# Performance work log

Hardware: AMD Instinct MI355X
Metric: run time of the kernel (lower is better)

Reference implementation:

```python
import jax, jax.numpy as jnp
import numpy as np

D_MODEL = 512
D_KEY = 512
D_VALUE = 512
DEG = 2                      # poly_degree
C = 16                       # context_window
D_POLY = (DEG + 1) * D_KEY   # 1536
MAX_NORM = 50.0
EPS = 1e-6
BATCH, SEQ = 8, 2048


def poly_features(x, coeffs):
    # phi(x) = concat_i coeffs[i] * x**i, i = 0..DEG   [..., (DEG+1)*d]
    outs = []
    xp = jnp.ones_like(x)
    for i in range(DEG + 1):
        outs.append(coeffs[i] * xp)
        xp = xp * x
    return jnp.concatenate(outs, axis=-1)


def _xavier(key, shape):
    fan_in, fan_out = shape[1], shape[0]
    lim = np.sqrt(6.0 / (fan_in + fan_out))
    return jax.random.uniform(key, shape, jnp.float32, -lim, lim)


def _logit(p):
    return float(np.log(p / (1.0 - p)))


def setup_inputs() -> dict:
    key = jax.random.key(0)
    ks = jax.random.split(key, 12)
    x = jax.random.normal(ks[0], (BATCH, SEQ, D_MODEL), jnp.float32)
    M0 = jnp.zeros((BATCH, D_POLY, D_VALUE), jnp.float32)
    S0 = jnp.zeros((BATCH, D_POLY, D_VALUE), jnp.float32)
    coeffs = jnp.array([1.0, 1.0, 0.5], jnp.float32)  # 1/i!
    return {
        "x": x, "M0": M0, "S0": S0,
        "Wk": _xavier(ks[1], (D_KEY, D_MODEL)),
        "Wv": _xavier(ks[2], (D_VALUE, D_MODEL)),
        "Wq": _xavier(ks[3], (D_KEY, D_MODEL)),
        "Wqk": jnp.eye(D_KEY, dtype=jnp.float32),
        "Wout": _xavier(ks[4], (D_MODEL, D_VALUE)),
        "coeffs": coeffs,
        "cgWq": _xavier(ks[5], (D_MODEL, D_MODEL)),
        "cgWk": _xavier(ks[6], (D_MODEL, D_MODEL)),
        "temp": jnp.ones((1,), jnp.float32),
        "aw": 0.01 * jax.random.normal(ks[7], (1, D_MODEL), jnp.float32),
        "ab": jnp.full((1,), _logit(0.99), jnp.float32),
        "tw": 0.01 * jax.random.normal(ks[8], (1, D_MODEL), jnp.float32),
        "tb": jnp.full((1,), _logit(0.9), jnp.float32),
        "ew": 0.01 * jax.random.normal(ks[9], (1, D_MODEL), jnp.float32),
        "eb": jnp.full((1,), _logit(0.1), jnp.float32),
    }


def _forward(x, M0, S0, Wk, Wv, Wq, Wqk, Wout, coeffs,
             cgWq, cgWk, temp, aw, ab, tw, tb, ew, eb):
    B, S, _ = x.shape
    n_chunks = S // C
    xc = x.reshape(B, n_chunks, C, D_MODEL).transpose(1, 0, 2, 3)  # [n,B,C,d]
    inv_temp = 1.0 / (D_MODEL ** 0.5 * jnp.maximum(temp[0], 0.1))

    def step(carry, chunk):
        M, Smom = carry                       # [B, d_poly, d_value]
        k = chunk @ Wk.T                      # [B,C,d_key]
        phi = poly_features(k, coeffs)        # [B,C,d_poly]
        v = chunk @ Wv.T                      # [B,C,d_value]
        # context gates from the current (last) token of the chunk
        qg = chunk[:, -1] @ cgWq.T            # [B,d]
        kg = chunk @ cgWk.T                   # [B,C,d]
        gamma = jax.nn.sigmoid(jnp.einsum('bcd,bd->bc', kg, qg) * inv_temp)
        # input-dependent alpha/theta/eta (mean-pooled chunk)
        xm = chunk.mean(axis=1)               # [B,d]
        alpha = jax.nn.sigmoid(xm @ aw.T + ab)[:, :, None]  # [B,1,1]
        theta = jax.nn.sigmoid(xm @ tw.T + tb)[:, :, None]
        eta = jax.nn.sigmoid(xm @ ew.T + eb)[:, :, None]
        # omega gradient: 2/C * Phi^T (Gamma (Phi M - V))
        pred = jnp.einsum('bcp,bpv->bcv', phi, M)
        err = gamma[..., None] * (pred - v)
        grad = (2.0 / C) * jnp.einsum('bcp,bcv->bpv', phi, err)
        S_new = theta * Smom - eta * grad
        M_new = alpha * M + S_new
        norms = jnp.sqrt(jnp.sum(M_new * M_new, axis=(-2, -1), keepdims=True))
        M_new = M_new * jnp.minimum(MAX_NORM / (norms + EPS), 1.0)
        # memory updates are detached by design (online learning inside scan)
        M_new = jax.lax.stop_gradient(M_new)
        S_new = jax.lax.stop_gradient(S_new)
        # read with polynomial-expanded query
        q = (chunk @ Wq.T) @ Wqk.T
        phiq = poly_features(q, coeffs)
        y = jnp.einsum('bcp,bpv->bcv', phiq, M_new) @ Wout.T
        return (M_new, S_new), y

    (_, _), ys = jax.lax.scan(step, (M0, S0), xc)   # ys: [n,B,C,d_model]
    return ys.transpose(1, 0, 2, 3).reshape(B, S, D_MODEL)


def reference(x, M0, S0, Wk, Wv, Wq, Wqk, Wout, coeffs,
              cgWq, cgWk, temp, aw, ab, tw, tb, ew, eb):
    return _forward(x, M0, S0, Wk, Wv, Wq, Wqk, Wout, coeffs,
                    cgWq, cgWk, temp, aw, ab, tw, tb, ew, eb)
```

## Files before the change

### kernel.cpp

```cpp
#include <hip/hip_runtime.h>
#include <hip/hip_bf16.h>
#include <math.h>

typedef __attribute__((ext_vector_type(4))) float f32x4;
typedef __attribute__((ext_vector_type(8))) short bf16x8;
typedef unsigned short u16;
typedef unsigned int u32;
typedef unsigned long long u64;

__device__ __forceinline__ float bf2f(u16 h){
  u32 u = ((u32)h) << 16;
  return __builtin_bit_cast(float, u);
}
__device__ __forceinline__ u16 f2bf(float f){
  u32 u = __builtin_bit_cast(u32, f);
  u32 r = (u + 0x7FFFu + ((u >> 16) & 1u)) >> 16;
  return (u16)r;
}
__device__ __forceinline__ float ldany(const void* p, long i, int f32){
  return f32 ? ((const float*)p)[i] : bf2f(((const u16*)p)[i]);
}

#define MFMA16(A, B, C) __builtin_amdgcn_mfma_f32_16x16x32_bf16(A, B, C, 0, 0, 0)
#define MM6(acc, AH, AM, AL, BH, BM, BL) \
  acc = MFMA16(AH, BH, acc); acc = MFMA16(AH, BM, acc); acc = MFMA16(AM, BH, acc); \
  acc = MFMA16(AM, BM, acc); acc = MFMA16(AL, BH, acc); acc = MFMA16(AH, BL, acc);

__global__ void detect_kernel(const u32* __restrict__ wqk_raw, int* __restrict__ flag){
  *flag = (wqk_raw[0] == 0x3F800000u) ? 1 : 0;
}

__global__ __launch_bounds__(512) void cvt_scalars_kernel(
    const void* temp, const void* aw, const void* ab, const void* tw, const void* tb,
    const void* ew, const void* eb, const void* coeffs, float* __restrict__ scal,
    const int* __restrict__ flag){
  int f = *flag; int d = threadIdx.x;
  scal[1 + d]    = ldany(aw, d, f);
  scal[514 + d]  = ldany(tw, d, f);
  scal[1027 + d] = ldany(ew, d, f);
  if (d == 0){
    scal[0]    = ldany(temp, 0, f);
    scal[513]  = ldany(ab, 0, f);
    scal[1026] = ldany(tb, 0, f);
    scal[1539] = ldany(eb, 0, f);
    scal[1540] = ldany(coeffs, 0, f);
    scal[1541] = ldany(coeffs, 1, f);
    scal[1542] = ldany(coeffs, 2, f);
  }
}

__global__ __launch_bounds__(256) void trans_kernel(
    const void* __restrict__ W, float* __restrict__ WT, const int* __restrict__ flag){
  int f = *flag;
  int idx = blockIdx.x * 256 + threadIdx.x;
  WT[idx] = ldany(W, (long)(idx & 511) * 512 + (idx >> 9), f);
}

__global__ __launch_bounds__(256) void split_kernel(
    const void* __restrict__ src, int srcmode, long n,
    u16* __restrict__ h, u16* __restrict__ m, u16* __restrict__ l,
    const int* __restrict__ flag){
  long i = (long)blockIdx.x * 256 + threadIdx.x;
  if (i >= n) return;
  int f = srcmode ? 1 : *flag;
  float v = ldany(src, i, f);
  u16 a = f2bf(v); float r1 = v - bf2f(a);
  u16 bq = f2bf(r1);
  h[i] = a; m[i] = bq; l[i] = f2bf(r1 - bf2f(bq));
}

__global__ __launch_bounds__(256) void gemm6(
    const u16* __restrict__ Ah, const u16* __restrict__ Am, const u16* __restrict__ Al,
    long a_off, int a_stride,
    const u16* __restrict__ Bh, const u16* __restrict__ Bm, const u16* __restrict__ Bl,
    void* __restrict__ OUT, int out_stride, int out_mode, const int* __restrict__ flag)
{
  const int rt = blockIdx.x;
  const int w = threadIdx.x >> 6, lane = threadIdx.x & 63;
  const int lm = lane & 15, quad = lane >> 4;
  const int col0 = blockIdx.y * 64 + w * 16;
  const long abase = a_off + (long)(rt * 16 + lm) * a_stride + quad * 8;
  const long bbase = (long)(col0 + lm) * 512 + quad * 8;
  f32x4 acc = {0.f, 0.f, 0.f, 0.f};
#pragma unroll
  for (int kk = 0; kk < 16; kk++){
    bf16x8 AH = *(const bf16x8*)(Ah + abase + kk * 32);
    bf16x8 AM = *(const bf16x8*)(Am + abase + kk * 32);
    bf16x8 AL = *(const bf16x8*)(Al + abase + kk * 32);
    bf16x8 BH = *(const bf16x8*)(Bh + bbase + kk * 32);
    bf16x8 BM = *(const bf16x8*)(Bm + bbase + kk * 32);
    bf16x8 BL = *(const bf16x8*)(Bl + bbase + kk * 32);
    MM6(acc, AH, AM, AL, BH, BM, BL)
  }
  const int orow = rt * 16 + quad * 4;
  const int f32out = (out_mode == 1) ? 1 : *flag;
#pragma unroll
  for (int r = 0; r < 4; r++){
    long o = (long)(orow + r) * out_stride + col0 + lm;
    if (f32out) ((float*)OUT)[o] = acc[r];
    else        ((u16*)OUT)[o]   = f2bf(acc[r]);
  }
}

__global__ __launch_bounds__(256) void gemm6s(
    const u16* __restrict__ Ah, const u16* __restrict__ Am, const u16* __restrict__ Al,
    long a_off, int a_stride,
    const u16* __restrict__ Bh, const u16* __restrict__ Bm, const u16* __restrict__ Bl,
    void* __restrict__ OUT, int out_stride, int out_mode,
    int rows_band, int cg, const int* __restrict__ flag)
{
  const int id = blockIdx.x;
  const int xcd = id & 7;
  const int s = id >> 3;
  const int per_grp = rows_band * cg;
  const int cgi = s / per_grp;
  const int t = s - cgi * per_grp;
  const int rt = xcd * rows_band + t / cg;
  const int ct = cgi * cg + (t - (t / cg) * cg);

  const int w = threadIdx.x >> 6, lane = threadIdx.x & 63;
  const int lm = lane & 15, quad = lane >> 4;
  const int col0 = ct * 64 + w * 16;
  const long abase = a_off + (long)(rt * 16 + lm) * a_stride + quad * 8;
  const long bbase = (long)(col0 + lm) * 512 + quad * 8;
  f32x4 acc = {0.f, 0.f, 0.f, 0.f};
#pragma unroll
  for (int kk = 0; kk < 16; kk++){
    bf16x8 AH = *(const bf16x8*)(Ah + abase + kk * 32);
    bf16x8 AM = *(const bf16x8*)(Am + abase + kk * 32);
    bf16x8 AL = *(const bf16x8*)(Al + abase + kk * 32);
    bf16x8 BH = *(const bf16x8*)(Bh + bbase + kk * 32);
    bf16x8 BM = *(const bf16x8*)(Bm + bbase + kk * 32);
    bf16x8 BL = *(const bf16x8*)(Bl + bbase + kk * 32);
    MM6(acc, AH, AM, AL, BH, BM, BL)
  }
  const int orow = rt * 16 + quad * 4;
  const int f32out = (out_mode == 1) ? 1 : *flag;
#pragma unroll
  for (int r = 0; r < 4; r++){
    long o = (long)(orow + r) * out_stride + col0 + lm;
    if (f32out) ((float*)OUT)[o] = acc[r];
    else        ((u16*)OUT)[o]   = f2bf(acc[r]);
  }
}

__global__ __launch_bounds__(256) void gamma_ate_kernel(
    const void* __restrict__ x, const float* __restrict__ z,
    const float* __restrict__ scal, const int* __restrict__ flag,
    float* __restrict__ gammaO, float* __restrict__ ateO)
{
  int bn = blockIdx.x;
  int tid = threadIdx.x;
  int f = *flag;
  __shared__ float gred[16][17];
  __shared__ float red[256];

  float t0 = scal[0];
  float mt = t0 > 0.1f ? t0 : 0.1f;
  float it = 1.0f / (22.627416997969522f * mt);

  int c = tid >> 4, part = tid & 15;
  long xrb = ((long)bn * 16 + c) * 512 + part * 32;
  const float* zr = z + (long)bn * 512 + part * 32;
  float p = 0.f;
  for (int e = 0; e < 32; e++) p += ldany(x, xrb + e, f) * zr[e];
  gred[c][part] = p;
  __syncthreads();
  if (tid < 16){
    float s = 0.f;
    for (int q2 = 0; q2 < 16; q2++) s += gred[tid][q2];
    gammaO[bn * 16 + tid] = 1.f / (1.f + expf(-it * s));
  }

  long xbase = (long)bn * 16 * 512;
  int d = tid * 2;
  float x0 = 0.f, x1 = 0.f;
  for (int cc = 0; cc < 16; cc++){
    x0 += ldany(x, xbase + cc * 512 + d, f);
    x1 += ldany(x, xbase + cc * 512 + d + 1, f);
  }
  x0 *= 0.0625f; x1 *= 0.0625f;
  float pa = x0 * scal[1 + d]    + x1 * scal[1 + d + 1];
  float pt = x0 * scal[514 + d]  + x1 * scal[514 + d + 1];
  float pe = x0 * scal[1027 + d] + x1 * scal[1027 + d + 1];

  red[tid] = pa; __syncthreads();
  for (int o = 128; o > 0; o >>= 1){ if (tid < o) red[tid] += red[tid + o]; __syncthreads(); }
  if (tid == 0) ateO[bn * 3 + 0] = 1.f / (1.f + expf(-(red[0] + scal[513])));
  __syncthreads();
  red[tid] = pt; __syncthreads();
  for (int o = 128; o > 0; o >>= 1){ if (tid < o) red[tid] += red[tid + o]; __syncthreads(); }
  if (tid == 0) ateO[bn * 3 + 1] = 1.f / (1.f + expf(-(red[0] + scal[1026])));
  __syncthreads();
  red[tid] = pe; __syncthreads();
  for (int o = 128; o > 0; o >>= 1){ if (tid < o) red[tid] += red[tid + o]; __syncthreads(); }
  if (tid == 0) ateO[bn * 3 + 2] = 1.f / (1.f + expf(-(red[0] + scal[1539])));
}

__device__ __forceinline__ void acc16f(const float4* k4, float c1M, float c2M,
                                       float pp[16]){
  float4 a = k4[0], b = k4[1], c = k4[2], d = k4[3];
  float kv[16] = {a.x,a.y,a.z,a.w, b.x,b.y,b.z,b.w, c.x,c.y,c.z,c.w, d.x,d.y,d.z,d.w};
#pragma unroll
  for (int i = 0; i < 16; i++){
    float t = c1M + kv[i] * c2M;
    pp[i] += kv[i] * t;
  }
}
__device__ __forceinline__ void grad16(const float4* k4, const float er[16],
                                       float& g1, float& g2){
  float4 a = k4[0], b = k4[1], c = k4[2], d = k4[3];
  float kv[16] = {a.x,a.y,a.z,a.w, b.x,b.y,b.z,b.w, c.x,c.y,c.z,c.w, d.x,d.y,d.z,d.w};
  float s1a = 0.f, s1b = 0.f, s2a = 0.f, s2b = 0.f;
#pragma unroll
  for (int i = 0; i < 16; i += 2){
    float ta = kv[i] * er[i];
    float tb = kv[i + 1] * er[i + 1];
    s1a += ta; s1b += tb;
    s2a += kv[i] * ta; s2b += kv[i + 1] * tb;
  }
  g1 = s1a + s1b; g2 = s2a + s2b;
}

__global__ __launch_bounds__(512, 2) void scan_kernel(
    const float* __restrict__ KVQ,
    const float* __restrict__ gammaA, const float* __restrict__ ateA,
    const float* __restrict__ scal,
    const void* __restrict__ M0, const void* __restrict__ S0,
    const int* __restrict__ flag,
    float* __restrict__ YT, u64* ssE)
{
  const int b = blockIdx.x >> 5;
  const int jt = blockIdx.x & 31, j0 = jt * 16;
  const int tid = threadIdx.x;
  const int g = tid >> 4, j = tid & 15, col = j0 + j;
  const int w = tid >> 6, lane = tid & 63;

  __shared__ float bufQ[512 * 16];
  __shared__ float bufK[512 * 16];
  __shared__ float redY[256 * 33];
  __shared__ float redP[256 * 33];
  __shared__ float errL[16 * 17];
  __shared__ float sprevS;
  __shared__ float ssw[8];

  const float c0f = scal[1540], c1f = scal[1541], c2f = scal[1542];
  const int f = *flag;

  float M[48], S[48];
  if (f){
#pragma unroll
    for (int k = 0; k < 48; k++){
      long gi = ((long)(b * 1536 + (k >> 4) * 512 + g + 32 * (k & 15))) * 512 + col;
      M[k] = ((const float*)M0)[gi];
      S[k] = ((const float*)S0)[gi];
    }
  } else {
#pragma unroll
    for (int k = 0; k < 48; k++){
      long gi = ((long)(b * 1536 + (k >> 4) * 512 + g + 32 * (k & 15))) * 512 + col;
      M[k] = bf2f(((const u16*)M0)[gi]);
      S[k] = bf2f(((const u16*)S0)[gi]);
    }
  }

  const int cS = tid & 15;
  const int dS = (tid >> 4) * 16;

  float4 k0, k1, k2, k3, q0, q1, q2, q3;
  {
    const float* ks = KVQ + ((long)(b * 2048 + cS)) * 1536 + dS;
    k0 = *(const float4*)(ks);     k1 = *(const float4*)(ks + 4);
    k2 = *(const float4*)(ks + 8); k3 = *(const float4*)(ks + 12);
  }
  q0 = k0; q1 = k1; q2 = k2; q3 = k3;

#pragma unroll 1
  for (int n = 0; n <= 128; n++){
    if (n > 0){
      float* bp = &bufQ[dS * 16 + cS];
      bp[0]   = q0.x; bp[16]  = q0.y; bp[32]  = q0.z; bp[48]  = q0.w;
      bp[64]  = q1.x; bp[80]  = q1.y; bp[96]  = q1.z; bp[112] = q1.w;
      bp[128] = q2.x; bp[144] = q2.y; bp[160] = q2.z; bp[176] = q2.w;
      bp[192] = q3.x; bp[208] = q3.y; bp[224] = q3.z; bp[240] = q3.w;
    }
    if (n < 128){
      float* bp = &bufK[dS * 16 + cS];
      bp[0]   = k0.x; bp[16]  = k0.y; bp[32]  = k0.z; bp[48]  = k0.w;
      bp[64]  = k1.x; bp[80]  = k1.y; bp[96]  = k1.z; bp[112] = k1.w;
      bp[128] = k2.x; bp[144] = k2.y; bp[160] = k2.z; bp[176] = k2.w;
      bp[192] = k3.x; bp[208] = k3.y; bp[224] = k3.z; bp[240] = k3.w;
    }
    __syncthreads();

    float vv = 0.f, gam = 0.f, alpha = 0.f, theta = 0.f, eta = 0.f;
    if (n < 128){
      const float* qs = KVQ + ((long)(b * 2048 + n * 16 + cS)) * 1536 + 1024 + dS;
      q0 = *(const float4*)(qs);     q1 = *(const float4*)(qs + 4);
      q2 = *(const float4*)(qs + 8); q3 = *(const float4*)(qs + 12);
      if (n < 127){
        const float* ks = KVQ + ((long)(b * 2048 + (n + 1) * 16 + cS)) * 1536 + dS;
        k0 = *(const float4*)(ks);     k1 = *(const float4*)(ks + 4);
        k2 = *(const float4*)(ks + 8); k3 = *(const float4*)(ks + 12);
      }
      if (tid >= 256){
        int idx = tid - 256, c2 = idx >> 4, j2 = idx & 15;
        vv  = KVQ[((long)(b * 2048 + n * 16 + c2)) * 1536 + 512 + j0 + j2];
        gam = gammaA[(b * 128 + n) * 16 + c2];
      }
      alpha = ateA[(b * 128 + n) * 3 + 0];
      theta = ateA[(b * 128 + n) * 3 + 1];
      eta   = ateA[(b * 128 + n) * 3 + 2];
    }

    float bsum = 0.f;
#pragma unroll
    for (int m = 0; m < 16; m++) bsum += M[m];
    const float base0 = c0f * bsum;

    {
      float pp[16];
#pragma unroll
      for (int c = 0; c < 16; c++) pp[c] = 0.f;
#pragma unroll
      for (int m = 0; m < 16; m++)
        acc16f((const float4*)&bufQ[g * 16 + m * 512],
               c1f * M[16 + m], c2f * M[32 + m], pp);
#pragma unroll
      for (int c = 0; c < 16; c++)
        redY[(c * 16 + j) * 33 + g] = base0 + pp[c];
    }
    {
      float pp[16];
#pragma unroll
      for (int c = 0; c < 16; c++) pp[c] = 0.f;
#pragma unroll
      for (int m = 0; m < 16; m++)
        acc16f((const float4*)&bufK[g * 16 + m * 512],
               c1f * M[16 + m], c2f * M[32 + m], pp);
#pragma unroll
      for (int c = 0; c < 16; c++)
        redP[(c * 16 + j) * 33 + g] = base0 + pp[c];
    }

    if (n > 0 && tid < 64){
      float ssv = 0.f;
      if (tid < 32){
        const u64* sp = ssE + ((n - 1) & 1) * 256 + b * 32;
        u64 v;
        for (;;){
          v = __hip_atomic_load(&sp[tid], __ATOMIC_RELAXED, __HIP_MEMORY_SCOPE_AGENT);
          if ((u32)(v >> 32) >= (u32)n) break;
          __builtin_amdgcn_s_sleep(1);
        }
        ssv = __builtin_bit_cast(float, (u32)(v & 0xFFFFFFFFu));
      }
#pragma unroll
      for (int o = 16; o > 0; o >>= 1) ssv += __shfl_xor(ssv, o);
      if (tid == 0) sprevS = fminf(50.0f / (sqrtf(ssv) + 1e-6f), 1.0f);
    }
    __syncthreads();
    const float s_prev = (n > 0) ? sprevS : 1.0f;

    if (tid < 256){
      if (n > 0){
        int c2 = tid >> 4, j2 = tid & 15;
        const float* rp = &redY[(c2 * 16 + j2) * 33];
        float yt = 0.f;
#pragma unroll
        for (int i = 0; i < 32; i++) yt += rp[i];
        YT[((long)(b * 2048 + (n - 1) * 16 + c2)) * 512 + j0 + j2] = s_prev * yt;
      }
    } else {
      if (n < 128){
        int idx = tid - 256, c2 = idx >> 4, j2 = idx & 15;
        const float* rp = &redP[(c2 * 16 + j2) * 33];
        float pred = 0.f;
#pragma unroll
        for (int i = 0; i < 32; i++) pred += rp[i];
        errL[c2 * 17 + j2] = 0.125f * gam * (s_prev * pred - vv);
      }
    }
    __syncthreads();

    if (n < 128){
      const float alphaS = alpha * s_prev;
      float er[16];
#pragma unroll
      for (int c = 0; c < 16; c++) er[c] = errL[c * 17 + j];
      float g0 = 0.f;
#pragma unroll
      for (int c = 0; c < 16; c++) g0 += er[c];
      float lss = 0.f;
#pragma unroll
      for (int m = 0; m < 16; m++){
        float g1, g2;
        grad16((const float4*)&bufK[g * 16 + m * 512], er, g1, g2);
        float sn1 = theta * S[16 + m] - eta * (c1f * g1);
        float an1 = alphaS * M[16 + m] + sn1;
        S[16 + m] = sn1; M[16 + m] = an1; lss += an1 * an1;
        float sn2 = theta * S[32 + m] - eta * (c2f * g2);
        float an2 = alphaS * M[32 + m] + sn2;
        S[32 + m] = sn2; M[32 + m] = an2; lss += an2 * an2;
      }
      float gv0 = eta * (c0f * g0);
#pragma unroll
      for (int m = 0; m < 16; m++){
        float sn = theta * S[m] - gv0;
        float an = alphaS * M[m] + sn;
        S[m] = sn; M[m] = an; lss += an * an;
      }
#pragma unroll
      for (int off2 = 32; off2 > 0; off2 >>= 1) lss += __shfl_down(lss, off2);
      if (lane == 0) ssw[w] = lss;
    }
    __syncthreads();
    if (n < 128 && tid == 0){
      float tot = ssw[0] + ssw[1] + ssw[2] + ssw[3]
                + ssw[4] + ssw[5] + ssw[6] + ssw[7];
      u64 pv = ((u64)(u32)(n + 1) << 32) | (u64)__builtin_bit_cast(u32, tot);
      __hip_atomic_store(&ssE[(n & 1) * 256 + b * 32 + jt], pv,
                         __ATOMIC_RELAXED, __HIP_MEMORY_SCOPE_AGENT);
    }
  }
}

extern "C" void kernel_launch(void* const* d_in, const int* in_sizes, int n_in,
                              void* d_out, int out_size, void* d_ws, size_t ws_size,
                              hipStream_t stream)
{
  (void)in_sizes; (void)n_in; (void)out_size;
  const void* x      = d_in[0];
  const void* M0     = d_in[1];
  const void* S0     = d_in[2];
  const void* Wk     = d_in[3];
  const void* Wv     = d_in[4];
  const void* Wq     = d_in[5];
  const void* Wqk    = d_in[6];
  const void* Wout   = d_in[7];
  const void* coeffs = d_in[8];
  const void* cgWq   = d_in[9];
  const void* cgWk   = d_in[10];
  const void* temp   = d_in[11];
  const void* aw     = d_in[12];
  const void* ab     = d_in[13];
  const void* tw     = d_in[14];
  const void* tb     = d_in[15];
  const void* ew     = d_in[16];
  const void* eb     = d_in[17];

  char* ws = (char*)d_ws;
  size_t off = 0;
  float* KVQ32 = (float*)(ws + off); off += 100663296;
  char*  XR  = ws + off;           off += 50331648;
  u16* Wsp   = (u16*)(ws + off);   off += 9437184;
  float* qg32  = (float*)(ws + off); off += 2097152;
  u16*   qgs   = (u16*)(ws + off);   off += 3145728;
  float* Wq2f  = (float*)(ws + off); off += 1048576;
  float* cgWkT = (float*)(ws + off); off += 1048576;
  float* z32   = (float*)(ws + off); off += 2097152;
  float* scal_  = (float*)(ws + off); off += 8192;
  float* gamma_ = (float*)(ws + off); off += 65536;
  float* ate_   = (float*)(ws + off); off += 12288;
  u64* ssE_     = (u64*)(ws + off); off += 4096;
  int* flag_    = (int*)(ws + off); off += 256;
  if (ws_size < off) return;

  u16* Xh = (u16*)XR;           u16* Xm = Xh + 8388608;  u16* Xl = Xm + 8388608;
  float* YT32 = (float*)XR;

  u16* Bqkvh = Wsp;             u16* Bqkvm = Wsp + 786432; u16* Bqkvl = Wsp + 1572864;
  u16* Wkh  = Bqkvh;            u16* Wvh  = Bqkvh + 262144; u16* Wq2h = Bqkvh + 524288;
  u16* Wkm  = Bqkvm;            u16* Wvm  = Bqkvm + 262144; u16* Wq2m = Bqkvm + 524288;
  u16* Wkl  = Bqkvl;            u16* Wvl  = Bqkvl + 262144; u16* Wq2l = Bqkvl + 524288;
  u16* cWqh = Wsp + 2359296;    u16* cWqm = cWqh + 262144; u16* cWql = cWqm + 262144;
  u16* cWkh = cWql + 262144;    u16* cWkm = cWkh + 262144; u16* cWkl = cWkm + 262144;
  u16* Woh  = cWkl + 262144;    u16* Wom  = Woh + 262144;  u16* Wol  = Wom + 262144;
  float* WqT32 = qg32;
  u16* Aqh = qgs;               u16* Aqm = Aqh + 262144;   u16* Aql = Aqm + 262144;
  u16* BqTh = Aql + 262144;     u16* BqTm = BqTh + 262144; u16* BqTl = BqTm + 262144;
  u16* qgh = qgs;               u16* qgm = qgh + 524288;   u16* qgl = qgm + 524288;
  u16* YTh = (u16*)KVQ32;       u16* YTm = YTh + 8388608;  u16* YTl = YTm + 8388608;

  detect_kernel<<<1, 1, 0, stream>>>((const u32*)Wqk, flag_);
  hipMemsetAsync(ssE_, 0, 4096, stream);
  cvt_scalars_kernel<<<1, 512, 0, stream>>>(temp, aw, ab, tw, tb, ew, eb, coeffs,
                                            scal_, flag_);
  trans_kernel<<<1024, 256, 0, stream>>>(cgWk, cgWkT, flag_);
  trans_kernel<<<1024, 256, 0, stream>>>(Wq, WqT32, flag_);

  split_kernel<<<32768, 256, 0, stream>>>(x,     0, 8388608L, Xh,  Xm,  Xl,  flag_);
  split_kernel<<<1024, 256, 0, stream>>>(Wk,    0, 262144L, Wkh,  Wkm,  Wkl,  flag_);
  split_kernel<<<1024, 256, 0, stream>>>(Wv,    0, 262144L, Wvh,  Wvm,  Wvl,  flag_);
  split_kernel<<<1024, 256, 0, stream>>>(Wqk,   0, 262144L, Aqh,  Aqm,  Aql,  flag_);
  split_kernel<<<1024, 256, 0, stream>>>(WqT32, 1, 262144L, BqTh, BqTm, BqTl, flag_);
  gemm6<<<dim3(32, 8), 256, 0, stream>>>(Aqh, Aqm, Aql, 0, 512,
                                         BqTh, BqTm, BqTl, Wq2f, 512, 1, flag_);
  split_kernel<<<1024, 256, 0, stream>>>(Wq2f,  1, 262144L, Wq2h, Wq2m, Wq2l, flag_);
  split_kernel<<<1024, 256, 0, stream>>>(cgWq,  0, 262144L, cWqh, cWqm, cWql, flag_);
  split_kernel<<<1024, 256, 0, stream>>>(cgWkT, 1, 262144L, cWkh, cWkm, cWkl, flag_);
  split_kernel<<<1024, 256, 0, stream>>>(Wout,  0, 262144L, Woh,  Wom,  Wol,  flag_);

  gemm6s<<<24576, 256, 0, stream>>>(Xh, Xm, Xl, 0, 512,
                                    Bqkvh, Bqkvm, Bqkvl, KVQ32, 1536, 1,
                                    128, 4, flag_);
  gemm6<<<dim3(64, 8), 256, 0, stream>>>(Xh, Xm, Xl, 15 * 512, 16 * 512,
                                         cWqh, cWqm, cWql, qg32, 512, 1, flag_);
  split_kernel<<<2048, 256, 0, stream>>>(qg32, 1, 524288L, qgh, qgm, qgl, flag_);
  gemm6<<<dim3(64, 8), 256, 0, stream>>>(qgh, qgm, qgl, 0, 512,
                                         cWkh, cWkm, cWkl, z32, 512, 1, flag_);
  gamma_ate_kernel<<<1024, 256, 0, stream>>>(x, z32, scal_, flag_, gamma_, ate_);

  scan_kernel<<<256, 512, 0, stream>>>(KVQ32, gamma_, ate_, scal_,
                                       M0, S0, flag_, YT32, ssE_);

  split_kernel<<<32768, 256, 0, stream>>>(YT32, 1, 8388608L, YTh, YTm, YTl, flag_);
  gemm6s<<<8192, 256, 0, stream>>>(YTh, YTm, YTl, 0, 512,
                                   Woh, Wom, Wol, d_out, 512, 2,
                                   128, 8, flag_);
}
```

Baseline: 3.076 ms.

## Vectorize splits, fuse Y split into scan, 4-tile GEMM rows, shuffle reductions

The split kernel now processes four elements per thread with vector loads and stores. The scan kernel writes the bf16 hi/mid/lo split of its output directly, which removes a full-size fp32 round trip and a separate split launch. The big GEMMs compute four 16-row tiles per block, so each B fragment is reused four times and fewer blocks are launched. gamma_ate replaces its shared-memory tree reductions with wavefront shuffles. Holding four accumulators per block raises register pressure, and the scan output now reuses the X split buffers.

```diff
diff --git a/kernel.cpp b/kernel.cpp
--- a/kernel.cpp
+++ b/kernel.cpp
@@ -57,16 +57,29 @@
 }
 
 __global__ __launch_bounds__(256) void split_kernel(
-    const void* __restrict__ src, int srcmode, long n,
+    const void* __restrict__ src, int srcmode, long n4,
     u16* __restrict__ h, u16* __restrict__ m, u16* __restrict__ l,
     const int* __restrict__ flag){
   long i = (long)blockIdx.x * 256 + threadIdx.x;
-  if (i >= n) return;
+  if (i >= n4) return;
   int f = srcmode ? 1 : *flag;
-  float v = ldany(src, i, f);
-  u16 a = f2bf(v); float r1 = v - bf2f(a);
-  u16 bq = f2bf(r1);
-  h[i] = a; m[i] = bq; l[i] = f2bf(r1 - bf2f(bq));
+  float v0, v1, v2, v3;
+  if (f){
+    float4 t = ((const float4*)src)[i];
+    v0 = t.x; v1 = t.y; v2 = t.z; v3 = t.w;
+  } else {
+    ushort4 t = ((const ushort4*)src)[i];
+    v0 = bf2f(t.x); v1 = bf2f(t.y); v2 = bf2f(t.z); v3 = bf2f(t.w);
+  }
+  ushort4 ho, mo, lo;
+#define SPL1(vv, H, M, L) { u16 a_ = f2bf(vv); float r_ = (vv) - bf2f(a_); \
+  u16 b_ = f2bf(r_); H = a_; M = b_; L = f2bf(r_ - bf2f(b_)); }
+  SPL1(v0, ho.x, mo.x, lo.x)
+  SPL1(v1, ho.y, mo.y, lo.y)
+  SPL1(v2, ho.z, mo.z, lo.z)
+  SPL1(v3, ho.w, mo.w, lo.w)
+#undef SPL1
+  ((ushort4*)h)[i] = ho; ((ushort4*)m)[i] = mo; ((ushort4*)l)[i] = lo;
 }
 
 __global__ __launch_bounds__(256) void gemm6(
@@ -102,46 +115,78 @@
   }
 }
 
-__global__ __launch_bounds__(256) void gemm6s(
+__global__ __launch_bounds__(256) void gemm6x4(
     const u16* __restrict__ Ah, const u16* __restrict__ Am, const u16* __restrict__ Al,
     long a_off, int a_stride,
     const u16* __restrict__ Bh, const u16* __restrict__ Bm, const u16* __restrict__ Bl,
     void* __restrict__ OUT, int out_stride, int out_mode,
-    int rows_band, int cg, const int* __restrict__ flag)
+    int band_rq, int cg, const int* __restrict__ flag)
 {
   const int id = blockIdx.x;
   const int xcd = id & 7;
   const int s = id >> 3;
-  const int per_grp = rows_band * cg;
+  const int per_grp = band_rq * cg;
   const int cgi = s / per_grp;
   const int t = s - cgi * per_grp;
-  const int rt = xcd * rows_band + t / cg;
+  const int rq = xcd * band_rq + t / cg;
   const int ct = cgi * cg + (t - (t / cg) * cg);
 
   const int w = threadIdx.x >> 6, lane = threadIdx.x & 63;
   const int lm = lane & 15, quad = lane >> 4;
   const int col0 = ct * 64 + w * 16;
-  const long abase = a_off + (long)(rt * 16 + lm) * a_stride + quad * 8;
   const long bbase = (long)(col0 + lm) * 512 + quad * 8;
-  f32x4 acc = {0.f, 0.f, 0.f, 0.f};
+  const long a0 = a_off + (long)(rq * 64 + lm) * a_stride + quad * 8;
+  const long as16 = (long)16 * a_stride;
+  f32x4 acc0 = {0.f,0.f,0.f,0.f}, acc1 = {0.f,0.f,0.f,0.f};
+  f32x4 acc2 = {0.f,0.f,0.f,0.f}, acc3 = {0.f,0.f,0.f,0.f};
 #pragma unroll
   for (int kk = 0; kk < 16; kk++){
-    bf16x8 AH = *(const bf16x8*)(Ah + abase + kk * 32);
-    bf16x8 AM = *(const bf16x8*)(Am + abase + kk * 32);
-    bf16x8 AL = *(const bf16x8*)(Al + abase + kk * 32);
     bf16x8 BH = *(const bf16x8*)(Bh + bbase + kk * 32);
     bf16x8 BM = *(const bf16x8*)(Bm + bbase + kk * 32);
     bf16x8 BL = *(const bf16x8*)(Bl + bbase + kk * 32);
-    MM6(acc, AH, AM, AL, BH, BM, BL)
-  }
-  const int orow = rt * 16 + quad * 4;
+    {
+      const long ab = a0 + kk * 32;
+      bf16x8 AH = *(const bf16x8*)(Ah + ab);
+      bf16x8 AM = *(const bf16x8*)(Am + ab);
+      bf16x8 AL = *(const bf16x8*)(Al + ab);
+      MM6(acc0, AH, AM, AL, BH, BM, BL)
+    }
+    {
+      const long ab = a0 + as16 + kk * 32;
+      bf16x8 AH = *(const bf16x8*)(Ah + ab);
+      bf16x8 AM = *(const bf16x8*)(Am + ab);
+      bf16x8 AL = *(const bf16x8*)(Al + ab);
+      MM6(acc1, AH, AM, AL, BH, BM, BL)
+    }
+    {
+      const long ab = a0 + 2 * as16 + kk * 32;
+      bf16x8 AH = *(const bf16x8*)(Ah + ab);
+      bf16x8 AM = *(const bf16x8*)(Am + ab);
+      bf16x8 AL = *(const bf16x8*)(Al + ab);
+      MM6(acc2, AH, AM, AL, BH, BM, BL)
+    }
+    {
+      const long ab = a0 + 3 * as16 + kk * 32;
+      bf16x8 AH = *(const bf16x8*)(Ah + ab);
+      bf16x8 AM = *(const bf16x8*)(Am + ab);
+      bf16x8 AL = *(const bf16x8*)(Al + ab);
+      MM6(acc3, AH, AM, AL, BH, BM, BL)
+    }
+  }
   const int f32out = (out_mode == 1) ? 1 : *flag;
-#pragma unroll
-  for (int r = 0; r < 4; r++){
-    long o = (long)(orow + r) * out_stride + col0 + lm;
-    if (f32out) ((float*)OUT)[o] = acc[r];
-    else        ((u16*)OUT)[o]   = f2bf(acc[r]);
-  }
+#define STORE_TILE(ACC, TT) { \
+  const int orow = rq * 64 + (TT) * 16 + quad * 4; \
+  _Pragma("unroll") \
+  for (int r = 0; r < 4; r++){ \
+    long o = (long)(orow + r) * out_stride + col0 + lm; \
+    if (f32out) ((float*)OUT)[o] = ACC[r]; \
+    else        ((u16*)OUT)[o]   = f2bf(ACC[r]); \
+  } }
+  STORE_TILE(acc0, 0)
+  STORE_TILE(acc1, 1)
+  STORE_TILE(acc2, 2)
+  STORE_TILE(acc3, 3)
+#undef STORE_TILE
 }
 
 __global__ __launch_bounds__(256) void gamma_ate_kernel(
@@ -152,8 +197,8 @@
   int bn = blockIdx.x;
   int tid = threadIdx.x;
   int f = *flag;
-  __shared__ float gred[16][17];
-  __shared__ float red[256];
+  int lane = tid & 63, w = tid >> 6;
+  __shared__ float redw[12];
 
   float t0 = scal[0];
   float mt = t0 > 0.1f ? t0 : 0.1f;
@@ -163,38 +208,38 @@
   long xrb = ((long)bn * 16 + c) * 512 + part * 32;
   const float* zr = z + (long)bn * 512 + part * 32;
   float p = 0.f;
+#pragma unroll
   for (int e = 0; e < 32; e++) p += ldany(x, xrb + e, f) * zr[e];
-  gred[c][part] = p;
-  __syncthreads();
-  if (tid < 16){
-    float s = 0.f;
-    for (int q2 = 0; q2 < 16; q2++) s += gred[tid][q2];
-    gammaO[bn * 16 + tid] = 1.f / (1.f + expf(-it * s));
-  }
+  p += __shfl_xor(p, 1); p += __shfl_xor(p, 2);
+  p += __shfl_xor(p, 4); p += __shfl_xor(p, 8);
+  if (part == 0) gammaO[bn * 16 + c] = 1.f / (1.f + expf(-it * p));
 
   long xbase = (long)bn * 16 * 512;
   int d = tid * 2;
   float x0 = 0.f, x1 = 0.f;
+#pragma unroll
   for (int cc = 0; cc < 16; cc++){
     x0 += ldany(x, xbase + cc * 512 + d, f);
     x1 += ldany(x, xbase + cc * 512 + d + 1, f);
   }
   x0 *= 0.0625f; x1 *= 0.0625f;
-  float pa = x0 * scal[1 + d]    + x1 * scal[1 + d + 1];
-  float pt = x0 * scal[514 + d]  + x1 * scal[514 + d + 1];
-  float pe = x0 * scal[1027 + d] + x1 * scal[1027 + d + 1];
-
-  red[tid] = pa; __syncthreads();
-  for (int o = 128; o > 0; o >>= 1){ if (tid < o) red[tid] += red[tid + o]; __syncthreads(); }
-  if (tid == 0) ateO[bn * 3 + 0] = 1.f / (1.f + expf(-(red[0] + scal[513])));
+  float pa = x0 * scal[1 + d]    + x1 * scal[2 + d];
+  float pt = x0 * scal[514 + d]  + x1 * scal[515 + d];
+  float pe = x0 * scal[1027 + d] + x1 * scal[1028 + d];
+#pragma unroll
+  for (int o = 32; o > 0; o >>= 1){
+    pa += __shfl_down(pa, o);
+    pt += __shfl_down(pt, o);
+    pe += __shfl_down(pe, o);
+  }
+  if (lane == 0){ redw[w] = pa; redw[4 + w] = pt; redw[8 + w] = pe; }
   __syncthreads();
-  red[tid] = pt; __syncthreads();
-  for (int o = 128; o > 0; o >>= 1){ if (tid < o) red[tid] += red[tid + o]; __syncthreads(); }
-  if (tid == 0) ateO[bn * 3 + 1] = 1.f / (1.f + expf(-(red[0] + scal[1026])));
-  __syncthreads();
-  red[tid] = pe; __syncthreads();
-  for (int o = 128; o > 0; o >>= 1){ if (tid < o) red[tid] += red[tid + o]; __syncthreads(); }
-  if (tid == 0) ateO[bn * 3 + 2] = 1.f / (1.f + expf(-(red[0] + scal[1539])));
+  if (tid < 3){
+    const float bias = (tid == 0) ? scal[513] : (tid == 1 ? scal[1026] : scal[1539]);
+    float sum = redw[tid * 4] + redw[tid * 4 + 1]
+              + redw[tid * 4 + 2] + redw[tid * 4 + 3];
+    ateO[bn * 3 + tid] = 1.f / (1.f + expf(-(sum + bias)));
+  }
 }
 
 __device__ __forceinline__ void acc16f(const float4* k4, float c1M, float c2M,
@@ -228,7 +273,8 @@
     const float* __restrict__ scal,
     const void* __restrict__ M0, const void* __restrict__ S0,
     const int* __restrict__ flag,
-    float* __restrict__ YT, u64* ssE)
+    u16* __restrict__ YTh, u16* __restrict__ YTm, u16* __restrict__ YTl,
+    u64* ssE)
 {
   const int b = blockIdx.x >> 5;
   const int jt = blockIdx.x & 31, j0 = jt * 16;
@@ -369,7 +415,11 @@
         float yt = 0.f;
 #pragma unroll
         for (int i = 0; i < 32; i++) yt += rp[i];
-        YT[((long)(b * 2048 + (n - 1) * 16 + c2)) * 512 + j0 + j2] = s_prev * yt;
+        float ov = s_prev * yt;
+        long oi = ((long)(b * 2048 + (n - 1) * 16 + c2)) * 512 + j0 + j2;
+        u16 hh = f2bf(ov); float r1 = ov - bf2f(hh);
+        u16 mm = f2bf(r1);
+        YTh[oi] = hh; YTm[oi] = mm; YTl[oi] = f2bf(r1 - bf2f(mm));
       }
     } else {
       if (n < 128){
@@ -467,7 +517,7 @@
   if (ws_size < off) return;
 
   u16* Xh = (u16*)XR;           u16* Xm = Xh + 8388608;  u16* Xl = Xm + 8388608;
-  float* YT32 = (float*)XR;
+  u16* YTh = Xh;                u16* YTm = Xm;           u16* YTl = Xl;
 
   u16* Bqkvh = Wsp;             u16* Bqkvm = Wsp + 786432; u16* Bqkvl = Wsp + 1572864;
   u16* Wkh  = Bqkvh;            u16* Wvh  = Bqkvh + 262144; u16* Wq2h = Bqkvh + 524288;
@@ -480,7 +530,6 @@
   u16* Aqh = qgs;               u16* Aqm = Aqh + 262144;   u16* Aql = Aqm + 262144;
   u16* BqTh = Aql + 262144;     u16* BqTm = BqTh + 262144; u16* BqTl = BqTm + 262144;
   u16* qgh = qgs;               u16* qgm = qgh + 524288;   u16* qgl = qgm + 524288;
-  u16* YTh = (u16*)KVQ32;       u16* YTm = YTh + 8388608;  u16* YTl = YTm + 8388608;
 
   detect_kernel<<<1, 1, 0, stream>>>((const u32*)Wqk, flag_);
   hipMemsetAsync(ssE_, 0, 4096, stream);
@@ -489,33 +538,32 @@
   trans_kernel<<<1024, 256, 0, stream>>>(cgWk, cgWkT, flag_);
   trans_kernel<<<1024, 256, 0, stream>>>(Wq, WqT32, flag_);
 
-  split_kernel<<<32768, 256, 0, stream>>>(x,     0, 8388608L, Xh,  Xm,  Xl,  flag_);
-  split_kernel<<<1024, 256, 0, stream>>>(Wk,    0, 262144L, Wkh,  Wkm,  Wkl,  flag_);
-  split_kernel<<<1024, 256, 0, stream>>>(Wv,    0, 262144L, Wvh,  Wvm,  Wvl,  flag_);
-  split_kernel<<<1024, 256, 0, stream>>>(Wqk,   0, 262144L, Aqh,  Aqm,  Aql,  flag_);
-  split_kernel<<<1024, 256, 0, stream>>>(WqT32, 1, 262144L, BqTh, BqTm, BqTl, flag_);
+  split_kernel<<<8192, 256, 0, stream>>>(x,     0, 2097152L, Xh,  Xm,  Xl,  flag_);
+  split_kernel<<<256, 256, 0, stream>>>(Wk,    0, 65536L, Wkh,  Wkm,  Wkl,  flag_);
+  split_kernel<<<256, 256, 0, stream>>>(Wv,    0, 65536L, Wvh,  Wvm,  Wvl,  flag_);
+  split_kernel<<<256, 256, 0, stream>>>(Wqk,   0, 65536L, Aqh,  Aqm,  Aql,  flag_);
+  split_kernel<<<256, 256, 0, stream>>>(WqT32, 1, 65536L, BqTh, BqTm, BqTl, flag_);
   gemm6<<<dim3(32, 8), 256, 0, stream>>>(Aqh, Aqm, Aql, 0, 512,
                                          BqTh, BqTm, BqTl, Wq2f, 512, 1, flag_);
-  split_kernel<<<1024, 256, 0, stream>>>(Wq2f,  1, 262144L, Wq2h, Wq2m, Wq2l, flag_);
-  split_kernel<<<1024, 256, 0, stream>>>(cgWq,  0, 262144L, cWqh, cWqm, cWql, flag_);
-  split_kernel<<<1024, 256, 0, stream>>>(cgWkT, 1, 262144L, cWkh, cWkm, cWkl, flag_);
-  split_kernel<<<1024, 256, 0, stream>>>(Wout,  0, 262144L, Woh,  Wom,  Wol,  flag_);
-
-  gemm6s<<<24576, 256, 0, stream>>>(Xh, Xm, Xl, 0, 512,
+  split_kernel<<<256, 256, 0, stream>>>(Wq2f,  1, 65536L, Wq2h, Wq2m, Wq2l, flag_);
+  split_kernel<<<256, 256, 0, stream>>>(cgWq,  0, 65536L, cWqh, cWqm, cWql, flag_);
+  split_kernel<<<256, 256, 0, stream>>>(cgWkT, 1, 65536L, cWkh, cWkm, cWkl, flag_);
+  split_kernel<<<256, 256, 0, stream>>>(Wout,  0, 65536L, Woh,  Wom,  Wol,  flag_);
+
+  gemm6x4<<<6144, 256, 0, stream>>>(Xh, Xm, Xl, 0, 512,
                                     Bqkvh, Bqkvm, Bqkvl, KVQ32, 1536, 1,
-                                    128, 4, flag_);
+                                    32, 4, flag_);
   gemm6<<<dim3(64, 8), 256, 0, stream>>>(Xh, Xm, Xl, 15 * 512, 16 * 512,
                                          cWqh, cWqm, cWql, qg32, 512, 1, flag_);
-  split_kernel<<<2048, 256, 0, stream>>>(qg32, 1, 524288L, qgh, qgm, qgl, flag_);
+  split_kernel<<<512, 256, 0, stream>>>(qg32, 1, 131072L, qgh, qgm, qgl, flag_);
   gemm6<<<dim3(64, 8), 256, 0, stream>>>(qgh, qgm, qgl, 0, 512,
                                          cWkh, cWkm, cWkl, z32, 512, 1, flag_);
   gamma_ate_kernel<<<1024, 256, 0, stream>>>(x, z32, scal_, flag_, gamma_, ate_);
 
   scan_kernel<<<256, 512, 0, stream>>>(KVQ32, gamma_, ate_, scal_,
-                                       M0, S0, flag_, YT32, ssE_);
-
-  split_kernel<<<32768, 256, 0, stream>>>(YT32, 1, 8388608L, YTh, YTm, YTl, flag_);
-  gemm6s<<<8192, 256, 0, stream>>>(YTh, YTm, YTl, 0, 512,
-                                   Woh, Wom, Wol, d_out, 512, 2,
-                                   128, 8, flag_);
-}
+                                       M0, S0, flag_, YTh, YTm, YTl, ssE_);
+
+  gemm6x4<<<2048, 256, 0, stream>>>(YTh, YTm, YTl, 0, 512,
+                                    Woh, Wom, Wol, d_out, 512, 2,
+                                    32, 8, flag_);
+}
```

Measured after the change: 2.476 ms. 1.24x faster.
